# Kernel optimization log

Hardware: AMD Instinct MI355X
Metric: run time of the kernel (lower is better)

The kernel has to match this reference:

```python
import jax, jax.numpy as jnp
import numpy as np

# TT-matrix dense layer: y = relu(x @ M + b) where M is a TT-matrix with cores
# G_k of shape [r_{k-1}, m_k, n_k, r_k], M[i1..id, j1..jd] = G1[:,i1,j1,:] ... Gd[:,id,jd,:]

IN_DIMS = [8, 8, 8, 8]
OUT_DIMS = [8, 8, 8, 8]
RANKS = [1, 8, 8, 8, 1]
BATCH = 4096


def setup_inputs() -> dict:
    key = jax.random.key(0)
    ks = jax.random.split(key, 6)
    inp = {"x": jax.random.normal(ks[0], (BATCH, int(np.prod(IN_DIMS))), dtype=jnp.float32)}
    # glorot-ish scale for TT cores so that the reconstructed matrix has sane variance
    for k in range(4):
        shape = (RANKS[k], IN_DIMS[k], OUT_DIMS[k], RANKS[k + 1])
        scale = 0.3
        inp[f"core{k}"] = scale * jax.random.normal(ks[1 + k], shape, dtype=jnp.float32)
    inp["b"] = 0.1 * jnp.ones((int(np.prod(OUT_DIMS)),), dtype=jnp.float32)
    return inp


def _tt_matmul(x, cores):
    # x: [B, prod(m)], cores[k]: [r_{k-1}, m_k, n_k, r_k]
    B = x.shape[0]
    ms = [G.shape[1] for G in cores]
    # res: [a, r, m_k, t] with a = B * prod(n_done), t = prod(m_rest)
    res = x.reshape(B, 1, ms[0], -1)
    for k, G in enumerate(cores):
        a, _, _, t = res.shape
        n, r_next = G.shape[2], G.shape[3]
        # contract rank and current input mode: [a, n, r_next, t]
        res = jnp.einsum('aqmt,qmnr->anrt', res, G)
        m_next = ms[k + 1] if k + 1 < len(cores) else 1
        res = res.reshape(a * n, r_next, m_next, t // m_next)
    return res.reshape(B, -1)  # [B, prod(n)], big-endian output index order


def reference(x, core0, core1, core2, core3, b):
    y = _tt_matmul(x, [core0, core1, core2, core3])
    return jax.nn.relu(y + b)
```

## Files before the change

kernel.cpp:

```cpp
#include <hip/hip_runtime.h>
#include <hip/hip_bf16.h>
#include <stdint.h>

typedef short bf16x8 __attribute__((ext_vector_type(8)));
typedef float f32x4 __attribute__((ext_vector_type(4)));
typedef unsigned short u16;
typedef u16 ushort8 __attribute__((ext_vector_type(8)));

typedef __attribute__((address_space(3))) void lds_void;
typedef const __attribute__((address_space(1))) void gbl_void;

#define BAR() do { asm volatile("" ::: "memory"); __builtin_amdgcn_s_barrier(); asm volatile("" ::: "memory"); } while (0)
#define WAITV(N) asm volatile("s_waitcnt vmcnt(" #N ")" ::: "memory")

__device__ __forceinline__ u16 f2bf(float f) {
  uint32_t u = __builtin_bit_cast(uint32_t, f);
  u += 0x7fffu + ((u >> 16) & 1u);
  return (u16)(u >> 16);
}

__global__ __launch_bounds__(256) void cvt_x(const float* __restrict__ x,
                                             u16* __restrict__ xb) {
  const int i = (blockIdx.x * 256 + threadIdx.x) * 8;
  float4 a = *(const float4*)(x + i);
  float4 b = *(const float4*)(x + i + 4);
  ushort8 o;
  o[0] = f2bf(a.x); o[1] = f2bf(a.y); o[2] = f2bf(a.z); o[3] = f2bf(a.w);
  o[4] = f2bf(b.x); o[5] = f2bf(b.y); o[6] = f2bf(b.z); o[7] = f2bf(b.w);
  *(ushort8*)(xb + i) = o;
}

__global__ __launch_bounds__(256) void build_mt(
    const float* __restrict__ c0, const float* __restrict__ c1,
    const float* __restrict__ c2, const float* __restrict__ c3,
    u16* __restrict__ Mt) {
  const int bid = blockIdx.x;
  const int j1 = bid & 7, i1 = (bid >> 3) & 7, j0 = (bid >> 6) & 7, i0 = bid >> 9;
  const int t = threadIdx.x;
  __shared__ float v[512];
  __shared__ float g3[512];
  g3[t] = c3[t];
  g3[t + 256] = c3[t + 256];
  float w2[8];
#pragma unroll
  for (int r2 = 0; r2 < 8; ++r2) {
    float s = 0.f;
#pragma unroll
    for (int r1 = 0; r1 < 8; ++r1)
      s += c0[(i0 * 8 + j0) * 8 + r1] * c1[((r1 * 8 + i1) * 8 + j1) * 8 + r2];
    w2[r2] = s;
  }
#pragma unroll
  for (int e = t; e < 512; e += 256) {
    const int r3 = e & 7, j2 = (e >> 3) & 7, i2 = e >> 6;
    float s = 0.f;
#pragma unroll
    for (int r2 = 0; r2 < 8; ++r2)
      s += w2[r2] * c2[((r2 * 8 + i2) * 8 + j2) * 8 + r3];
    v[e] = s;
  }
  __syncthreads();
  const int jr = t >> 2, ic0 = (t & 3) * 16;
  const int j2 = jr >> 3, j3 = jr & 7;
  const size_t base =
      (size_t)(j0 * 512 + j1 * 64 + jr) * 4096 + (i0 * 512 + i1 * 64) + ic0;
  ushort8 o0, o1;
#pragma unroll
  for (int q = 0; q < 16; ++q) {
    const int ic = ic0 + q, i2 = ic >> 3, i3 = ic & 7;
    float s = 0.f;
#pragma unroll
    for (int r3 = 0; r3 < 8; ++r3)
      s += v[(i2 << 6) + (j2 << 3) + r3] * g3[(r3 << 6) + (i3 << 3) + j3];
    const u16 h = f2bf(s);
    if (q < 8) o0[q] = h; else o1[q - 8] = h;
  }
  *(ushort8*)(Mt + base) = o0;
  *(ushort8*)(Mt + base + 8) = o1;
}

__global__ __launch_bounds__(512, 2) void gemm_bias_relu(
    const u16* __restrict__ A, const u16* __restrict__ Bt,
    const float* __restrict__ bias, float* __restrict__ C) {
  constexpr int K = 4096, N = 4096, NT = 64;
  __shared__ __align__(16) char lds[131072];
  const int t = threadIdx.x;
  const int l = t & 63, w = t >> 6;
  const int wr = w >> 2, wc = w & 3;
  const int lr = l & 15, lk = l >> 4;

  const int id = blockIdx.x;
  const int wg = (id & 7) * 32 + (id >> 3);
  const int bm = wg >> 4, bn = wg & 15;

  const char* gA = (const char*)A + (size_t)bm * 256 * (K * 2);
  const char* gB = (const char*)Bt + (size_t)bn * 256 * (K * 2);
  const int srow = t >> 3;
  const int schunk = (t & 7) ^ (srow & 7);
  const int sgo = srow * (K * 2) + schunk * 16;
  const int sld = t * 16;

  const int axor = (lk ^ (lr & 7)) * 16;
  const int aoff0 = (wr * 128 + lr) * 128 + axor;
  const int aoff1 = aoff0 ^ 64;
  const int boff0 = 65536 + (wc * 64 + lr) * 128 + axor;
  const int boff1 = boff0 ^ 64;

  auto stA = [&](int p, int h, int kt) {
    const char* src = gA + (size_t)(h * 128) * (K * 2) + kt * 128 + sgo;
    char* dst = lds + p * 32768 + h * 16384 + sld;
    __builtin_amdgcn_global_load_lds((gbl_void*)src, (lds_void*)dst, 16, 0, 0);
    __builtin_amdgcn_global_load_lds((gbl_void*)(src + (size_t)64 * (K * 2)),
                                     (lds_void*)(dst + 8192), 16, 0, 0);
  };
  auto stB = [&](int p, int h, int kt) {
    const char* src = gB + (size_t)(h * 128) * (K * 2) + kt * 128 + sgo;
    char* dst = lds + 65536 + p * 32768 + h * 16384 + sld;
    __builtin_amdgcn_global_load_lds((gbl_void*)src, (lds_void*)dst, 16, 0, 0);
    __builtin_amdgcn_global_load_lds((gbl_void*)(src + (size_t)64 * (K * 2)),
                                     (lds_void*)(dst + 8192), 16, 0, 0);
  };
  auto rdA = [&](int p, int off, int m) -> bf16x8 {
    return *(const bf16x8*)(lds + p * 32768 + off + m * 2048);
  };
  auto rdB = [&](int p, int off, int n) -> bf16x8 {
    return *(const bf16x8*)(lds + p * 32768 + off + n * 2048);
  };

  bf16x8 a0[8], a1[8], b01[2][2], b23[2][2];
  f32x4 acc[8][4];
#pragma unroll
  for (int m = 0; m < 8; ++m)
#pragma unroll
    for (int n = 0; n < 4; ++n) acc[m][n] = f32x4{0.f, 0.f, 0.f, 0.f};

  stA(0, 0, 0); stA(0, 1, 0); stB(0, 0, 0); stB(0, 1, 0);
  stA(1, 0, 1); stA(1, 1, 1); stB(1, 0, 1); stB(1, 1, 1);
  WAITV(8);
  BAR();
#pragma unroll
  for (int m = 0; m < 8; ++m) a0[m] = rdA(0, aoff0, m);
#pragma unroll
  for (int n = 0; n < 2; ++n) { b01[n][0] = rdB(0, boff0, n); b01[n][1] = rdB(0, boff1, n); }

  for (int it = 0; it < NT / 2; ++it) {
#pragma unroll
    for (int hf = 0; hf < 2; ++hf) {
      const int p = hf;
      const int kt = 2 * it + hf;
      const int kn = (kt + 2 < NT) ? kt + 2 : kt;
#pragma unroll
      for (int m = 0; m < 8; ++m) a1[m] = rdA(p, aoff1, m);
      BAR();
      __builtin_amdgcn_s_setprio(1);
#pragma unroll
      for (int m = 0; m < 8; ++m)
#pragma unroll
        for (int n = 0; n < 2; ++n)
          acc[m][n] = __builtin_amdgcn_mfma_f32_16x16x32_bf16(a0[m], b01[n][0], acc[m][n], 0, 0, 0);
      __builtin_amdgcn_s_setprio(0);
      BAR();
#pragma unroll
      for (int n = 0; n < 2; ++n) { b23[n][0] = rdB(p, boff0, n + 2); b23[n][1] = rdB(p, boff1, n + 2); }
      stA(p, 0, kn); stA(p, 1, kn);
      BAR();
      __builtin_amdgcn_s_setprio(1);
#pragma unroll
      for (int m = 0; m < 8; ++m)
#pragma unroll
        for (int n = 0; n < 2; ++n)
          acc[m][n] = __builtin_amdgcn_mfma_f32_16x16x32_bf16(a1[m], b01[n][1], acc[m][n], 0, 0, 0);
      __builtin_amdgcn_s_setprio(0);
      WAITV(4);
      BAR();
#pragma unroll
      for (int n = 0; n < 2; ++n) { b01[n][0] = rdB(p ^ 1, boff0, n); b01[n][1] = rdB(p ^ 1, boff1, n); }
      stB(p, 0, kn); stB(p, 1, kn);
      BAR();
      __builtin_amdgcn_s_setprio(1);
#pragma unroll
      for (int m = 0; m < 8; ++m)
#pragma unroll
        for (int n = 0; n < 2; ++n)
          acc[m][2 + n] = __builtin_amdgcn_mfma_f32_16x16x32_bf16(a0[m], b23[n][0], acc[m][2 + n], 0, 0, 0);
      __builtin_amdgcn_s_setprio(0);
      BAR();
#pragma unroll
      for (int m = 0; m < 8; ++m) a0[m] = rdA(p ^ 1, aoff0, m);
      BAR();
      __builtin_amdgcn_s_setprio(1);
#pragma unroll
      for (int m = 0; m < 8; ++m)
#pragma unroll
        for (int n = 0; n < 2; ++n)
          acc[m][2 + n] = __builtin_amdgcn_mfma_f32_16x16x32_bf16(a1[m], b23[n][1], acc[m][2 + n], 0, 0, 0);
      __builtin_amdgcn_s_setprio(0);
      BAR();
    }
  }

  const int row0 = bm * 256 + wr * 128;
  const int col0 = bn * 256 + wc * 64;
#pragma unroll
  for (int n = 0; n < 4; ++n) {
    const int col = col0 + n * 16 + lr;
    const float bv = bias[col];
#pragma unroll
    for (int m = 0; m < 8; ++m) {
      const int r0 = row0 + m * 16 + lk * 4;
#pragma unroll
      for (int vv = 0; vv < 4; ++vv) {
        const float val = acc[m][n][vv] + bv;
        C[(size_t)(r0 + vv) * N + col] = val > 0.f ? val : 0.f;
      }
    }
  }
}

extern "C" void kernel_launch(void* const* d_in, const int* in_sizes, int n_in,
                              void* d_out, int out_size, void* d_ws, size_t ws_size,
                              hipStream_t stream) {
  const float* x  = (const float*)d_in[0];
  const float* c0 = (const float*)d_in[1];
  const float* c1 = (const float*)d_in[2];
  const float* c2 = (const float*)d_in[3];
  const float* c3 = (const float*)d_in[4];
  const float* b  = (const float*)d_in[5];
  float* out = (float*)d_out;

  u16* xb  = (u16*)d_ws;
  u16* mtb = xb + (size_t)4096 * 4096;

  cvt_x<<<dim3(16777216 / (256 * 8)), dim3(256), 0, stream>>>(x, xb);
  build_mt<<<dim3(4096), dim3(256), 0, stream>>>(c0, c1, c2, c3, mtb);
  gemm_bias_relu<<<dim3(256), dim3(512), 0, stream>>>(xb, mtb, b, out);
}
```

Measured before the change: 149.6 us.

## Restructure GEMM main loop into quadrant-based MFMA schedule with staggered loads

Rewrites the GEMM inner loop so each K tile is processed as four quadrant MFMA blocks (M-half by N-half, both K halves), with LDS fragment reads and global-to-LDS prefetches interleaved between quadrants and explicit lgkmcnt/vmcnt waits. The aim is better overlap of LDS reads and global loads with matrix core work and fewer register fragment sets. It also drops the XCD-aware block remapping in favour of a plain 2D grid, which may change L2 locality across chiplets. The tighter hand-scheduled waits risk stalls or races if the vmcnt counts are off.

Measured after the change: 144.6 us. 3.4% less time.

```diff
diff --git a/kernel.cpp b/kernel.cpp
--- a/kernel.cpp
+++ b/kernel.cpp
@@ -12,6 +12,8 @@
 
 #define BAR() do { asm volatile("" ::: "memory"); __builtin_amdgcn_s_barrier(); asm volatile("" ::: "memory"); } while (0)
 #define WAITV(N) asm volatile("s_waitcnt vmcnt(" #N ")" ::: "memory")
+#define WAITL0() do { asm volatile("s_waitcnt lgkmcnt(0)" ::: "memory"); __builtin_amdgcn_sched_barrier(0); } while (0)
+#define HINTL8() asm volatile("s_waitcnt lgkmcnt(8)" ::: "memory")
 
 __device__ __forceinline__ u16 f2bf(float f) {
   uint32_t u = __builtin_bit_cast(uint32_t, f);
@@ -88,10 +90,7 @@
   const int l = t & 63, w = t >> 6;
   const int wr = w >> 2, wc = w & 3;
   const int lr = l & 15, lk = l >> 4;
-
-  const int id = blockIdx.x;
-  const int wg = (id & 7) * 32 + (id >> 3);
-  const int bm = wg >> 4, bn = wg & 15;
+  const int bm = blockIdx.y, bn = blockIdx.x;
 
   const char* gA = (const char*)A + (size_t)bm * 256 * (K * 2);
   const char* gB = (const char*)Bt + (size_t)bn * 256 * (K * 2);
@@ -127,77 +126,92 @@
     return *(const bf16x8*)(lds + p * 32768 + off + n * 2048);
   };
 
-  bf16x8 a0[8], a1[8], b01[2][2], b23[2][2];
+  bf16x8 aH0[8], aH1[8], bH0[4], bH1[4];
   f32x4 acc[8][4];
 #pragma unroll
   for (int m = 0; m < 8; ++m)
 #pragma unroll
     for (int n = 0; n < 4; ++n) acc[m][n] = f32x4{0.f, 0.f, 0.f, 0.f};
 
-  stA(0, 0, 0); stA(0, 1, 0); stB(0, 0, 0); stB(0, 1, 0);
-  stA(1, 0, 1); stA(1, 1, 1); stB(1, 0, 1); stB(1, 1, 1);
-  WAITV(8);
+  auto rdAH = [&](bf16x8* d, int p, int mh) {
+#pragma unroll
+    for (int m2 = 0; m2 < 4; ++m2) {
+      d[m2 * 2 + 0] = rdA(p, aoff0, mh * 4 + m2);
+      d[m2 * 2 + 1] = rdA(p, aoff1, mh * 4 + m2);
+    }
+  };
+  auto rdBH = [&](bf16x8* d, int p, int nh) {
+#pragma unroll
+    for (int n2 = 0; n2 < 2; ++n2) {
+      d[n2 * 2 + 0] = rdB(p, boff0, nh * 2 + n2);
+      d[n2 * 2 + 1] = rdB(p, boff1, nh * 2 + n2);
+    }
+  };
+  auto quad = [&](int mh, int nh, bf16x8* aH, bf16x8* bH) {
+    __builtin_amdgcn_s_setprio(1);
+#pragma unroll
+    for (int kk = 0; kk < 2; ++kk)
+#pragma unroll
+      for (int m2 = 0; m2 < 4; ++m2)
+#pragma unroll
+        for (int n2 = 0; n2 < 2; ++n2)
+          acc[mh * 4 + m2][nh * 2 + n2] = __builtin_amdgcn_mfma_f32_16x16x32_bf16(
+              aH[m2 * 2 + kk], bH[n2 * 2 + kk], acc[mh * 4 + m2][nh * 2 + n2], 0, 0, 0);
+    __builtin_amdgcn_s_setprio(0);
+  };
+
+  stA(0, 0, 0); stB(0, 0, 0); stB(0, 1, 0); stA(0, 1, 0);
+  stB(1, 0, 1); stB(1, 1, 1);
+  WAITV(4);
   BAR();
-#pragma unroll
-  for (int m = 0; m < 8; ++m) a0[m] = rdA(0, aoff0, m);
-#pragma unroll
-  for (int n = 0; n < 2; ++n) { b01[n][0] = rdB(0, boff0, n); b01[n][1] = rdB(0, boff1, n); }
 
   for (int it = 0; it < NT / 2; ++it) {
-#pragma unroll
-    for (int hf = 0; hf < 2; ++hf) {
-      const int p = hf;
-      const int kt = 2 * it + hf;
-      const int kn = (kt + 2 < NT) ? kt + 2 : kt;
-#pragma unroll
-      for (int m = 0; m < 8; ++m) a1[m] = rdA(p, aoff1, m);
-      BAR();
-      __builtin_amdgcn_s_setprio(1);
-#pragma unroll
-      for (int m = 0; m < 8; ++m)
-#pragma unroll
-        for (int n = 0; n < 2; ++n)
-          acc[m][n] = __builtin_amdgcn_mfma_f32_16x16x32_bf16(a0[m], b01[n][0], acc[m][n], 0, 0, 0);
-      __builtin_amdgcn_s_setprio(0);
-      BAR();
-#pragma unroll
-      for (int n = 0; n < 2; ++n) { b23[n][0] = rdB(p, boff0, n + 2); b23[n][1] = rdB(p, boff1, n + 2); }
-      stA(p, 0, kn); stA(p, 1, kn);
-      BAR();
-      __builtin_amdgcn_s_setprio(1);
-#pragma unroll
-      for (int m = 0; m < 8; ++m)
-#pragma unroll
-        for (int n = 0; n < 2; ++n)
-          acc[m][n] = __builtin_amdgcn_mfma_f32_16x16x32_bf16(a1[m], b01[n][1], acc[m][n], 0, 0, 0);
-      __builtin_amdgcn_s_setprio(0);
-      WAITV(4);
-      BAR();
-#pragma unroll
-      for (int n = 0; n < 2; ++n) { b01[n][0] = rdB(p ^ 1, boff0, n); b01[n][1] = rdB(p ^ 1, boff1, n); }
-      stB(p, 0, kn); stB(p, 1, kn);
-      BAR();
-      __builtin_amdgcn_s_setprio(1);
-#pragma unroll
-      for (int m = 0; m < 8; ++m)
-#pragma unroll
-        for (int n = 0; n < 2; ++n)
-          acc[m][2 + n] = __builtin_amdgcn_mfma_f32_16x16x32_bf16(a0[m], b23[n][0], acc[m][2 + n], 0, 0, 0);
-      __builtin_amdgcn_s_setprio(0);
-      BAR();
-#pragma unroll
-      for (int m = 0; m < 8; ++m) a0[m] = rdA(p ^ 1, aoff0, m);
-      BAR();
-      __builtin_amdgcn_s_setprio(1);
-#pragma unroll
-      for (int m = 0; m < 8; ++m)
-#pragma unroll
-        for (int n = 0; n < 2; ++n)
-          acc[m][2 + n] = __builtin_amdgcn_mfma_f32_16x16x32_bf16(a1[m], b23[n][1], acc[m][2 + n], 0, 0, 0);
-      __builtin_amdgcn_s_setprio(0);
-      BAR();
-    }
-  }
+    const int T = 2 * it;
+    const int t2 = (T + 2 < NT) ? T + 2 : NT - 1;
+    const int t3 = (T + 3 < NT) ? T + 3 : NT - 1;
+    rdAH(aH0, 0, 0); rdBH(bH0, 0, 0);
+    stA(1, 0, T + 1);
+    HINTL8();
+    BAR(); WAITL0();
+    quad(0, 0, aH0, bH0);
+    BAR();
+    rdBH(bH1, 0, 1);
+    stA(1, 1, T + 1);
+    BAR(); WAITL0();
+    quad(0, 1, aH0, bH1);
+    BAR();
+    rdAH(aH1, 0, 1);
+    stB(0, 0, t2);
+    BAR(); WAITL0();
+    quad(1, 1, aH1, bH1);
+    BAR();
+    stB(0, 1, t2); stA(0, 0, t2);
+    BAR(); WAITL0();
+    quad(1, 0, aH1, bH0);
+    WAITV(6);
+    BAR();
+    rdAH(aH0, 1, 0); rdBH(bH0, 1, 0);
+    stA(0, 1, t2);
+    HINTL8();
+    BAR(); WAITL0();
+    quad(0, 0, aH0, bH0);
+    BAR();
+    rdBH(bH1, 1, 1);
+    BAR(); WAITL0();
+    quad(0, 1, aH0, bH1);
+    BAR();
+    rdAH(aH1, 1, 1);
+    stB(1, 0, t3);
+    BAR(); WAITL0();
+    quad(1, 1, aH1, bH1);
+    BAR();
+    stB(1, 1, t3);
+    BAR(); WAITL0();
+    quad(1, 0, aH1, bH0);
+    WAITV(4);
+    BAR();
+  }
+  WAITV(0);
 
   const int row0 = bm * 256 + wr * 128;
   const int col0 = bn * 256 + wc * 64;
@@ -233,5 +247,5 @@
 
   cvt_x<<<dim3(16777216 / (256 * 8)), dim3(256), 0, stream>>>(x, xb);
   build_mt<<<dim3(4096), dim3(256), 0, stream>>>(c0, c1, c2, c3, mtb);
-  gemm_bias_relu<<<dim3(256), dim3(512), 0, stream>>>(xb, mtb, b, out);
-}
+  gemm_bias_relu<<<dim3(16, 16), dim3(512), 0, stream>>>(xb, mtb, b, out);
+}
```
